# Kernel tuning notes

Measured on AMD Instinct MI355X. Metric: run time of the kernel, lower is better.

The kernel has to match this reference:

```python
import jax, jax.numpy as jnp
import numpy as np

# --- quantization helpers (I-BERT-style symmetric quantization) ---

def _quant_int(x, scale, bit):
    # round(x/scale) clamped to signed `bit`-bit range (SymmetricQuantFunction)
    n = 2 ** (bit - 1) - 1
    return jnp.clip(jnp.round(x / scale), -n - 1, n)


def quant_linear(x, s_x, W, b, weight_bit=8):
    """QuantLinear: per-output-channel symmetric 8-bit weight quant, int GEMM, dequant.
    Returns (output, bias_scaling_factor[out_features])."""
    n = 2 ** (weight_bit - 1) - 1
    w_scale = jnp.maximum(jnp.max(jnp.abs(W), axis=1), 1e-8) / n          # (out,)
    w_int = _quant_int(W, w_scale[:, None], weight_bit)                   # int-valued (out,in)
    b_scale = w_scale * s_x                                               # (out,) broadcasts with scalar s_x
    b_int = jnp.round(b / b_scale)                                        # 32-bit bias, no clamp needed
    x_int = x / s_x                                                       # int-valued activations
    out_int = jnp.einsum('bsi,oi->bso', x_int, w_int) + b_int
    return out_int * b_scale, b_scale


def quant_act(x, bit):
    """QuantAct: per-tensor symmetric requantization to `bit` bits (dynamic min/max)."""
    n = 2 ** (bit - 1) - 1
    scale = jnp.maximum(jnp.max(jnp.abs(x)), 1e-8) / n                    # scalar
    x_int = _quant_int(x, scale, bit)
    return x_int * scale, scale


def int_gelu(x, s):
    """IntGELU (I-BERT): integer 2nd-order polynomial approximation of erf."""
    k = 1.4142
    c0, c1 = -0.2888, -1.769
    c2 = 1.0 / c0
    SHIFT = 14  # 'const' in the original code

    x_int = x / s
    se = s / k  # scaling factor fed to int_erf
    # --- int_erf ---
    b_int = jnp.floor(c1 / se)
    c_int = jnp.floor(c2 / se ** 2)
    sign = jnp.sign(x_int)
    abs_int = jnp.minimum(jnp.abs(x_int), -b_int)
    y_int = sign * ((abs_int + b_int) ** 2 + c_int)
    se2 = se ** 2 * c0
    y_int = jnp.floor(y_int / 2 ** SHIFT)
    se2 = se2 * 2 ** SHIFT
    # --- gelu = x * (erf/2 + 1/2) in integer form ---
    shift_int = jnp.floor(1.0 / se2)
    out_int = x_int * (y_int + shift_int)
    s_out = s * se2 / 2
    return out_int * s_out, s_out


def setup_inputs() -> dict:
    key = jax.random.key(0)
    k_x, k_w1, k_b1, k_w2, k_b2 = jax.random.split(key, 5)
    B, S, D, H = 8, 1024, 768, 3072
    x = jax.random.normal(k_x, (B, S, D), dtype=jnp.float32)
    act_scaling_factor = jnp.full((1,), 0.02, dtype=jnp.float32)
    # pre-quantize x onto its input grid (x arrives already quantized in the real pipeline)
    x = jnp.round(x / act_scaling_factor) * act_scaling_factor
    W1 = jax.random.normal(k_w1, (H, D), dtype=jnp.float32) * 0.02
    b1 = jax.random.normal(k_b1, (H,), dtype=jnp.float32) * 0.02
    W2 = jax.random.normal(k_w2, (D, H), dtype=jnp.float32) * 0.02
    b2 = jax.random.normal(k_b2, (D,), dtype=jnp.float32) * 0.02
    return {"x": x, "act_scaling_factor": act_scaling_factor,
            "W1": W1, "b1": b1, "W2": W2, "b2": b2}


def reference(x, act_scaling_factor, W1, b1, W2, b2):
    s = act_scaling_factor
    h, s = quant_linear(x, s, W1, b1)       # fc1: int8 GEMM + dequant
    h, s = quant_act(h, 8)                  # qact_gelu
    h, s = int_gelu(h, s)                   # IntGELU
    h, s = quant_act(h, 8)                  # qact1 (drop=0.0 -> identity)
    h, s = quant_linear(h, s, W2, b2)       # fc2
    h, s = quant_act(h, 16)                 # qact2 (16-bit)
    return h, s
```

## Files before the change

### kernel.cpp

```cpp
#include <hip/hip_runtime.h>

typedef _Float16 half8  __attribute__((ext_vector_type(8)));
typedef _Float16 half4v __attribute__((ext_vector_type(4)));
typedef float f32x4 __attribute__((ext_vector_type(4)));
typedef int int4v __attribute__((ext_vector_type(4)));

#define M_DIM 8192
#define D_DIM 768
#define H_DIM 3072

#define WS_WSCALE2   16
#define WS_BINT1     (WS_WSCALE2 + 768*4)
#define WS_BSCALE1   (WS_BINT1 + 3072*4)
#define WS_BINT2     (WS_BSCALE1 + 3072*4)
#define WS_BSCALE2   (WS_BINT2 + 768*4)
#define WS_XQ        34560UL
#define WS_WQ1       (WS_XQ  + (size_t)M_DIM*D_DIM*2)
#define WS_WQ2I      (WS_WQ1 + (size_t)H_DIM*D_DIM*2)
#define WS_H1        (WS_WQ2I + (size_t)D_DIM*H_DIM)
#define WS_Q2        WS_H1
#define WS_H2        (WS_H1 + (size_t)M_DIM*H_DIM)
#define WS_Q1        (WS_H1 + (size_t)M_DIM*H_DIM*4)

__device__ __forceinline__ void gl_lds16(const _Float16* g, _Float16* l) {
  __builtin_amdgcn_global_load_lds(
      (const __attribute__((address_space(1))) void*)g,
      (__attribute__((address_space(3))) void*)l, 16, 0, 0);
}
__device__ __forceinline__ void gl_lds16c(const char* g, char* l) {
  __builtin_amdgcn_global_load_lds(
      (const __attribute__((address_space(1))) void*)g,
      (__attribute__((address_space(3))) void*)l, 16, 0, 0);
}

struct GeluP { float scale1, bintg, cintg, shiftint, s_out; };

__device__ __forceinline__ GeluP gelu_params(float max1) {
  GeluP p;
  p.scale1 = fmaxf(max1, 1e-8f) / 127.0f;
  float se = p.scale1 / 1.4142f;
  p.bintg = floorf(-1.769f / se);
  p.cintg = floorf(((float)(1.0 / -0.2888)) / (se * se));
  float se2 = ((se * se) * -0.2888f) * 16384.0f;
  p.shiftint = floorf(1.0f / se2);
  p.s_out = (p.scale1 * se2) * 0.5f;
  return p;
}

__device__ __forceinline__ float gelu_val(const GeluP& p, float qf) {
  float sg = (qf > 0.f) ? 1.f : ((qf < 0.f) ? -1.f : 0.f);
  float aq = fminf(fabsf(qf), -p.bintg);
  float t = aq + p.bintg;
  float y = sg * (t * t + p.cintg);
  float yf = floorf(y * (1.0f / 16384.0f));
  return (qf * (yf + p.shiftint)) * p.s_out;
}

__global__ __launch_bounds__(256)
void k1_prep(const float* __restrict__ W1, const float* __restrict__ b1,
             const float* __restrict__ W2, const float* __restrict__ sxp,
             _Float16* __restrict__ wq1, char* __restrict__ wq2i,
             float* __restrict__ wscale2, float* __restrict__ bint1,
             float* __restrict__ bscale1, unsigned* __restrict__ wsu)
{
  if (blockIdx.x == 0 && threadIdx.x == 0) { wsu[0] = 0u; wsu[1] = 0u; wsu[2] = 0u; }
  int w = blockIdx.x * 4 + (threadIdx.x >> 6);
  int lane = threadIdx.x & 63;
  if (w < H_DIM) {
    const float* row = W1 + (size_t)w * D_DIM;
    f32x4 v[3]; float m = 0.f;
#pragma unroll
    for (int t = 0; t < 3; t++) {
      v[t] = *(const f32x4*)(row + t * 256 + lane * 4);
#pragma unroll
      for (int j = 0; j < 4; j++) m = fmaxf(m, fabsf(v[t][j]));
    }
#pragma unroll
    for (int off = 32; off >= 1; off >>= 1) m = fmaxf(m, __shfl_xor(m, off));
    float wsc = fmaxf(m, 1e-8f) / 127.0f;
    _Float16* orow = wq1 + (size_t)w * D_DIM;
#pragma unroll
    for (int t = 0; t < 3; t++) {
      half4v h;
#pragma unroll
      for (int j = 0; j < 4; j++) {
        float q = fminf(fmaxf(rintf(v[t][j] / wsc), -128.f), 127.f);
        h[j] = (_Float16)q;
      }
      *(half4v*)(orow + t * 256 + lane * 4) = h;
    }
    if (lane == 0) {
      float bs = wsc * sxp[0];
      bint1[w] = rintf(b1[w] / bs);
      bscale1[w] = bs;
    }
  } else {
    int o = w - H_DIM;
    const float* row = W2 + (size_t)o * H_DIM;
    f32x4 v[12]; float m = 0.f;
#pragma unroll
    for (int t = 0; t < 12; t++) {
      v[t] = *(const f32x4*)(row + t * 256 + lane * 4);
#pragma unroll
      for (int j = 0; j < 4; j++) m = fmaxf(m, fabsf(v[t][j]));
    }
#pragma unroll
    for (int off = 32; off >= 1; off >>= 1) m = fmaxf(m, __shfl_xor(m, off));
    float wsc = fmaxf(m, 1e-8f) / 127.0f;
    unsigned* orow = (unsigned*)(wq2i + (size_t)o * H_DIM);
#pragma unroll
    for (int t = 0; t < 12; t++) {
      unsigned pk = 0;
#pragma unroll
      for (int j = 0; j < 4; j++) {
        float q = fminf(fmaxf(rintf(v[t][j] / wsc), -128.f), 127.f);
        pk |= ((unsigned)(unsigned char)(char)(int)q) << (8 * j);
      }
      orow[t * 64 + lane] = pk;
    }
    if (lane == 0) wscale2[o] = wsc;
  }
}

__global__ __launch_bounds__(256)
void k2_quant_x(const float* __restrict__ x, const float* __restrict__ sxp,
                _Float16* __restrict__ xq, int n4)
{
  float sx = sxp[0];
  int stride = gridDim.x * blockDim.x;
  for (int i = blockIdx.x * blockDim.x + threadIdx.x; i < n4; i += stride) {
    f32x4 v = ((const f32x4*)x)[i];
    half4v h;
#pragma unroll
    for (int j = 0; j < 4; j++) h[j] = (_Float16)(v[j] / sx);
    ((half4v*)xq)[i] = h;
  }
}

#define SLOT_A 4096
#define SLOT_B 8192
#define SLOT_SZ (SLOT_A + SLOT_B)

__global__ __launch_bounds__(512)
void gemm_f16_dp(const _Float16* __restrict__ A, const _Float16* __restrict__ B,
                 const float* __restrict__ bint, const float* __restrict__ bscale,
                 float* __restrict__ C, unsigned* __restrict__ maxw, int N, int K)
{
  __shared__ _Float16 lds[3 * SLOT_SZ];
  __shared__ float wred[8];
  const int tid = threadIdx.x;
  const int wid = tid >> 6;
  const int lane = tid & 63;
  const int m0 = blockIdx.x * 128;
  const int n0 = blockIdx.y * 256;
  const int wm = wid >> 2;
  const int wn = wid & 3;

  const int sr = lane >> 2;
  const int sc = lane & 3;
  const int ra  = wid * 16 + sr;
  const int csa = sc ^ ((ra >> 1) & 3);
  const int rb  = wid * 16 + sr;
  const int csb = sc ^ ((rb >> 1) & 3);
  const _Float16* pa  = A + (size_t)(m0 + ra) * K + csa * 8;
  const _Float16* pb0 = B + (size_t)(n0 + rb) * K + csb * 8;
  const _Float16* pb1 = B + (size_t)(n0 + rb + 128) * K + csb * 8;
  _Float16* const da  = lds;
  _Float16* const db0 = lds + SLOT_A;
  _Float16* const db1 = lds + SLOT_A + 4096;

#define STAGE_DP(t, s) do {                                                  \
    const int _o = (s) * SLOT_SZ + wid * 512;                                \
    gl_lds16(pa  + (size_t)(t) * 32, da  + _o);                              \
    gl_lds16(pb0 + (size_t)(t) * 32, db0 + _o);                              \
    gl_lds16(pb1 + (size_t)(t) * 32, db1 + _o);                              \
  } while (0)

  int aoff[4], boff[4];
  const int ks = lane >> 4;
#pragma unroll
  for (int f = 0; f < 4; f++) {
    int r = wm * 64 + f * 16 + (lane & 15);
    aoff[f] = r * 64 + ((ks ^ ((r >> 1) & 3)) * 16);
    int rn = wn * 64 + f * 16 + (lane & 15);
    boff[f] = SLOT_A * 2 + rn * 64 + ((ks ^ ((rn >> 1) & 3)) * 16);
  }

  f32x4 acc[4][4];
#pragma unroll
  for (int i = 0; i < 4; i++)
#pragma unroll
    for (int j = 0; j < 4; j++) acc[i][j] = (f32x4){0.f, 0.f, 0.f, 0.f};

  const int nt = K / 32;
  STAGE_DP(0, 0);
  STAGE_DP(1, 1);
  for (int t = 0; t < nt; ++t) {
    const int s = t % 3;
    if (t + 1 < nt) asm volatile("s_waitcnt vmcnt(3)" ::: "memory");
    else            asm volatile("s_waitcnt vmcnt(0)" ::: "memory");
    asm volatile("s_barrier" ::: "memory");
    if (t + 2 < nt) STAGE_DP(t + 2, (t + 2) % 3);
    const char* sb = (const char*)(lds + s * SLOT_SZ);
    half8 a[4], b01[2], b23[2];
#pragma unroll
    for (int f = 0; f < 4; f++) a[f] = *(const half8*)(sb + aoff[f]);
    b01[0] = *(const half8*)(sb + boff[0]);
    b01[1] = *(const half8*)(sb + boff[1]);
    __builtin_amdgcn_s_setprio(1);
#pragma unroll
    for (int i = 0; i < 4; i++)
#pragma unroll
      for (int j = 0; j < 2; j++)
        acc[i][j] = __builtin_amdgcn_mfma_f32_16x16x32_f16(a[i], b01[j], acc[i][j], 0, 0, 0);
    __builtin_amdgcn_s_setprio(0);
    b23[0] = *(const half8*)(sb + boff[2]);
    b23[1] = *(const half8*)(sb + boff[3]);
    __builtin_amdgcn_s_setprio(1);
#pragma unroll
    for (int i = 0; i < 4; i++)
#pragma unroll
      for (int j = 0; j < 2; j++)
        acc[i][j + 2] = __builtin_amdgcn_mfma_f32_16x16x32_f16(a[i], b23[j], acc[i][j + 2], 0, 0, 0);
    __builtin_amdgcn_s_setprio(0);
  }
#undef STAGE_DP

  float tmax = 0.f;
  const int orow0 = m0 + wm * 64 + (lane >> 4) * 4;
  const int ocol0 = n0 + wn * 64 + (lane & 15);
#pragma unroll
  for (int j = 0; j < 4; j++) {
    const int col = ocol0 + j * 16;
    const float bi = bint[col];
    const float bs = bscale[col];
#pragma unroll
    for (int i = 0; i < 4; i++) {
#pragma unroll
      for (int e = 0; e < 4; e++) {
        const int rowm = orow0 + i * 16 + e;
        float v = (acc[i][j][e] + bi) * bs;
        C[(size_t)rowm * N + col] = v;
        tmax = fmaxf(tmax, fabsf(v));
      }
    }
  }
#pragma unroll
  for (int off = 32; off >= 1; off >>= 1) tmax = fmaxf(tmax, __shfl_xor(tmax, off));
  if (lane == 0) wred[wid] = tmax;
  __syncthreads();
  if (tid == 0) {
    float bm = 0.f;
#pragma unroll
    for (int i = 0; i < 8; i++) bm = fmaxf(bm, wred[i]);
    atomicMax(maxw, __float_as_uint(bm));
  }
}

__global__ __launch_bounds__(256)
void k4_gelu(const float* __restrict__ h1, const unsigned* __restrict__ wsu,
             char* __restrict__ q1, unsigned* __restrict__ maxw, int n4)
{
  GeluP p = gelu_params(__uint_as_float(wsu[0]));
  float tmax = 0.f;
  int stride = gridDim.x * blockDim.x;
  for (int i = blockIdx.x * blockDim.x + threadIdx.x; i < n4; i += stride) {
    f32x4 h = ((const f32x4*)h1)[i];
    unsigned pack = 0;
#pragma unroll
    for (int j = 0; j < 4; j++) {
      float qf = fminf(fmaxf(rintf(h[j] / p.scale1), -128.f), 127.f);
      tmax = fmaxf(tmax, fabsf(gelu_val(p, qf)));
      pack |= ((unsigned)(unsigned char)(char)(int)qf) << (8 * j);
    }
    ((unsigned*)q1)[i] = pack;
  }
#pragma unroll
  for (int off = 32; off >= 1; off >>= 1) tmax = fmaxf(tmax, __shfl_xor(tmax, off));
  __shared__ float wred[4];
  int wid = threadIdx.x >> 6;
  if ((threadIdx.x & 63) == 0) wred[wid] = tmax;
  __syncthreads();
  if (threadIdx.x == 0) {
    float bm = fmaxf(fmaxf(wred[0], wred[1]), fmaxf(wred[2], wred[3]));
    atomicMax(maxw, __float_as_uint(bm));
  }
}

__global__ __launch_bounds__(256)
void k6_bias(const unsigned* __restrict__ wsu, const float* __restrict__ wscale2,
             const float* __restrict__ b2, float* __restrict__ bint2,
             float* __restrict__ bscale2)
{
  float scale2 = fmaxf(__uint_as_float(wsu[1]), 1e-8f) / 127.0f;
  for (int o = threadIdx.x; o < D_DIM; o += 256) {
    float bs = wscale2[o] * scale2;
    bint2[o] = rintf(b2[o] / bs);
    bscale2[o] = bs;
  }
}

__global__ __launch_bounds__(256)
void k5_q2(const char* __restrict__ q1, const unsigned* __restrict__ wsu,
           char* __restrict__ q2, int n16)
{
  GeluP p = gelu_params(__uint_as_float(wsu[0]));
  float scale2 = fmaxf(__uint_as_float(wsu[1]), 1e-8f) / 127.0f;
  int stride = gridDim.x * blockDim.x;
  for (int i = blockIdx.x * blockDim.x + threadIdx.x; i < n16; i += stride) {
    uint4 pk = ((const uint4*)q1)[i];
    uint4 o;
    unsigned* pw[4] = {&o.x, &o.y, &o.z, &o.w};
    unsigned pr[4] = {pk.x, pk.y, pk.z, pk.w};
#pragma unroll
    for (int w = 0; w < 4; w++) {
      unsigned acc = 0;
#pragma unroll
      for (int j = 0; j < 4; j++) {
        float qf = (float)(int)(signed char)(pr[w] >> (8 * j));
        float g = gelu_val(p, qf);
        float q2f = fminf(fmaxf(rintf(g / scale2), -128.f), 127.f);
        acc |= ((unsigned)(unsigned char)(char)(int)q2f) << (8 * j);
      }
      *pw[w] = acc;
    }
    ((uint4*)q2)[i] = o;
  }
}

#define I8_SLOT_A 8192
#define I8_SLOT_SZ (2 * I8_SLOT_A)

__global__ __launch_bounds__(256)
void gemm_i8_dp(const char* __restrict__ A, const char* __restrict__ B,
                const float* __restrict__ bint, const float* __restrict__ bscale,
                float* __restrict__ C, unsigned* __restrict__ maxw, int N, int K)
{
  __shared__ char lds[3 * I8_SLOT_SZ];
  __shared__ float wred[4];
  const int tid = threadIdx.x;
  const int wid = tid >> 6;
  const int lane = tid & 63;
  const int m0 = blockIdx.x * 128;
  const int n0 = blockIdx.y * 128;
  const int wm = wid >> 1;
  const int wn = wid & 1;

  const int rr = lane >> 2;
  const int c  = lane & 3;
  const int r0 = wid * 16 + rr;
  const int r1 = r0 + 64;
  const int c0 = c ^ (r0 & 3) ^ ((r0 >> 2) & 3);
  const int c1 = c ^ (r1 & 3) ^ ((r1 >> 2) & 3);
  const char* pa0 = A + (size_t)(m0 + r0) * K + c0 * 16;
  const char* pa1 = A + (size_t)(m0 + r1) * K + c1 * 16;
  const char* pb0 = B + (size_t)(n0 + r0) * K + c0 * 16;
  const char* pb1 = B + (size_t)(n0 + r1) * K + c1 * 16;

#define STAGE_I8(t, s) do {                                                   \
    char* const base = lds + (s) * I8_SLOT_SZ;                                \
    gl_lds16c(pa0 + (size_t)(t) * 64, base + wid * 1024);                     \
    gl_lds16c(pa1 + (size_t)(t) * 64, base + 4096 + wid * 1024);              \
    gl_lds16c(pb0 + (size_t)(t) * 64, base + I8_SLOT_A + wid * 1024);         \
    gl_lds16c(pb1 + (size_t)(t) * 64, base + I8_SLOT_A + 4096 + wid * 1024);  \
  } while (0)

  int aoff[4], boff[4];
  const int ks = lane >> 4;
#pragma unroll
  for (int f = 0; f < 4; f++) {
    int r = wm * 64 + f * 16 + (lane & 15);
    aoff[f] = r * 64 + ((ks ^ (r & 3) ^ ((r >> 2) & 3)) * 16);
    int rn = wn * 64 + f * 16 + (lane & 15);
    boff[f] = I8_SLOT_A + rn * 64 + ((ks ^ (rn & 3) ^ ((rn >> 2) & 3)) * 16);
  }

  int4v acc[4][4];
#pragma unroll
  for (int i = 0; i < 4; i++)
#pragma unroll
    for (int j = 0; j < 4; j++) acc[i][j] = (int4v){0, 0, 0, 0};

  const int nt = K / 64;
  STAGE_I8(0, 0);
  STAGE_I8(1, 1);
  for (int t = 0; t < nt; ++t) {
    const int s = t % 3;
    if (t + 1 < nt) asm volatile("s_waitcnt vmcnt(4)" ::: "memory");
    else            asm volatile("s_waitcnt vmcnt(0)" ::: "memory");
    asm volatile("s_barrier" ::: "memory");
    if (t + 2 < nt) STAGE_I8(t + 2, (t + 2) % 3);
    const char* sb = lds + s * I8_SLOT_SZ;
    int4v a[4], b01[2], b23[2];
#pragma unroll
    for (int f = 0; f < 4; f++) a[f] = *(const int4v*)(sb + aoff[f]);
    b01[0] = *(const int4v*)(sb + boff[0]);
    b01[1] = *(const int4v*)(sb + boff[1]);
    __builtin_amdgcn_s_setprio(1);
#pragma unroll
    for (int i = 0; i < 4; i++)
#pragma unroll
      for (int j = 0; j < 2; j++)
        acc[i][j] = __builtin_amdgcn_mfma_i32_16x16x64_i8(a[i], b01[j], acc[i][j], 0, 0, 0);
    __builtin_amdgcn_s_setprio(0);
    b23[0] = *(const int4v*)(sb + boff[2]);
    b23[1] = *(const int4v*)(sb + boff[3]);
    __builtin_amdgcn_s_setprio(1);
#pragma unroll
    for (int i = 0; i < 4; i++)
#pragma unroll
      for (int j = 0; j < 2; j++)
        acc[i][j + 2] = __builtin_amdgcn_mfma_i32_16x16x64_i8(a[i], b23[j], acc[i][j + 2], 0, 0, 0);
    __builtin_amdgcn_s_setprio(0);
  }
#undef STAGE_I8

  float tmax = 0.f;
  const int orow0 = m0 + wm * 64 + (lane >> 4) * 4;
  const int ocol0 = n0 + wn * 64 + (lane & 15);
#pragma unroll
  for (int j = 0; j < 4; j++) {
    const int col = ocol0 + j * 16;
    const float bi = bint[col];
    const float bs = bscale[col];
#pragma unroll
    for (int i = 0; i < 4; i++) {
#pragma unroll
      for (int e = 0; e < 4; e++) {
        const int rowm = orow0 + i * 16 + e;
        float v = ((float)acc[i][j][e] + bi) * bs;
        C[(size_t)rowm * N + col] = v;
        tmax = fmaxf(tmax, fabsf(v));
      }
    }
  }
#pragma unroll
  for (int off = 32; off >= 1; off >>= 1) tmax = fmaxf(tmax, __shfl_xor(tmax, off));
  if (lane == 0) wred[wid] = tmax;
  __syncthreads();
  if (tid == 0) {
    float bm = fmaxf(fmaxf(wred[0], wred[1]), fmaxf(wred[2], wred[3]));
    atomicMax(maxw, __float_as_uint(bm));
  }
}

__global__ __launch_bounds__(256)
void k7_final(const float* __restrict__ h2, const unsigned* __restrict__ wsu,
              float* __restrict__ out, int n4, int ntot)
{
  float scale16 = fmaxf(__uint_as_float(wsu[2]), 1e-8f) / 32767.0f;
  int stride = gridDim.x * blockDim.x;
  for (int i = blockIdx.x * blockDim.x + threadIdx.x; i < n4; i += stride) {
    f32x4 v = ((const f32x4*)h2)[i];
    f32x4 o;
#pragma unroll
    for (int j = 0; j < 4; j++) {
      float q = fminf(fmaxf(rintf(v[j] / scale16), -32768.f), 32767.f);
      o[j] = q * scale16;
    }
    ((f32x4*)out)[i] = o;
  }
  if (blockIdx.x == 0 && threadIdx.x == 0) out[ntot] = scale16;
}

extern "C" void kernel_launch(void* const* d_in, const int* in_sizes, int n_in,
                              void* d_out, int out_size, void* d_ws, size_t ws_size,
                              hipStream_t stream)
{
  (void)in_sizes; (void)n_in; (void)out_size; (void)ws_size;
  const float* x  = (const float*)d_in[0];
  const float* sx = (const float*)d_in[1];
  const float* W1 = (const float*)d_in[2];
  const float* b1 = (const float*)d_in[3];
  const float* W2 = (const float*)d_in[4];
  const float* b2 = (const float*)d_in[5];
  float* out = (float*)d_out;
  char* ws = (char*)d_ws;

  unsigned* wsu   = (unsigned*)ws;
  float* wscale2  = (float*)(ws + WS_WSCALE2);
  float* bint1    = (float*)(ws + WS_BINT1);
  float* bscale1  = (float*)(ws + WS_BSCALE1);
  float* bint2    = (float*)(ws + WS_BINT2);
  float* bscale2  = (float*)(ws + WS_BSCALE2);
  _Float16* xq    = (_Float16*)(ws + WS_XQ);
  _Float16* wq1   = (_Float16*)(ws + WS_WQ1);
  char* wq2i      = (char*)(ws + WS_WQ2I);
  float* h1       = (float*)(ws + WS_H1);
  char* q2        = (char*)(ws + WS_Q2);
  float* h2       = (float*)(ws + WS_H2);
  char* q1        = (char*)(ws + WS_Q1);

  k1_prep<<<dim3(960), dim3(256), 0, stream>>>(W1, b1, W2, sx, wq1, wq2i, wscale2, bint1, bscale1, wsu);
  k2_quant_x<<<dim3(2048), dim3(256), 0, stream>>>(x, sx, xq, (M_DIM * D_DIM) / 4);
  gemm_f16_dp<<<dim3(64, 12), dim3(512), 0, stream>>>(xq, wq1, bint1, bscale1, h1, wsu + 0, H_DIM, D_DIM);
  k4_gelu<<<dim3(2048), dim3(256), 0, stream>>>(h1, wsu, q1, wsu + 1, (M_DIM * H_DIM) / 4);
  k6_bias<<<dim3(1), dim3(256), 0, stream>>>(wsu, wscale2, b2, bint2, bscale2);
  k5_q2<<<dim3(2048), dim3(256), 0, stream>>>(q1, wsu, q2, (M_DIM * H_DIM) / 16);
  gemm_i8_dp<<<dim3(64, 6), dim3(256), 0, stream>>>(q2, wq2i, bint2, bscale2, h2, wsu + 2, D_DIM, H_DIM);
  k7_final<<<dim3(2048), dim3(256), 0, stream>>>(h2, wsu, out, (M_DIM * D_DIM) / 4, M_DIM * D_DIM);
}
```

Baseline: 183.4 us.

## Fuse GELU requant into int8 GEMM via LUT and merge prep kernels

Removes the separate q1->q2 requantization pass and the bias kernel by building a 256-entry GELU+requant lookup table per wave from shuffled registers. The second GEMM's A operand is loaded to registers, remapped through the table, and written to LDS, while B keeps the direct global-to-LDS path. The bias is computed in the epilogue, and the weight prep and x quantization kernels are merged into one launch. The GEMM tile shrinks to 64 rows to fit the register-staged A path, which doubles the grid but lowers per-block reuse of B and adds shuffle work to the inner loop.

```diff
diff --git a/kernel.cpp b/kernel.cpp
--- a/kernel.cpp
+++ b/kernel.cpp
@@ -12,13 +12,10 @@
 #define WS_WSCALE2   16
 #define WS_BINT1     (WS_WSCALE2 + 768*4)
 #define WS_BSCALE1   (WS_BINT1 + 3072*4)
-#define WS_BINT2     (WS_BSCALE1 + 3072*4)
-#define WS_BSCALE2   (WS_BINT2 + 768*4)
 #define WS_XQ        34560UL
 #define WS_WQ1       (WS_XQ  + (size_t)M_DIM*D_DIM*2)
 #define WS_WQ2I      (WS_WQ1 + (size_t)H_DIM*D_DIM*2)
 #define WS_H1        (WS_WQ2I + (size_t)D_DIM*H_DIM)
-#define WS_Q2        WS_H1
 #define WS_H2        (WS_H1 + (size_t)M_DIM*H_DIM)
 #define WS_Q1        (WS_H1 + (size_t)M_DIM*H_DIM*4)
 
@@ -57,83 +54,83 @@
 }
 
 __global__ __launch_bounds__(256)
-void k1_prep(const float* __restrict__ W1, const float* __restrict__ b1,
-             const float* __restrict__ W2, const float* __restrict__ sxp,
-             _Float16* __restrict__ wq1, char* __restrict__ wq2i,
-             float* __restrict__ wscale2, float* __restrict__ bint1,
-             float* __restrict__ bscale1, unsigned* __restrict__ wsu)
+void k12_prep(const float* __restrict__ W1, const float* __restrict__ b1,
+              const float* __restrict__ W2, const float* __restrict__ x,
+              const float* __restrict__ sxp,
+              _Float16* __restrict__ wq1, char* __restrict__ wq2i,
+              float* __restrict__ wscale2, float* __restrict__ bint1,
+              float* __restrict__ bscale1, _Float16* __restrict__ xq,
+              unsigned* __restrict__ wsu)
 {
   if (blockIdx.x == 0 && threadIdx.x == 0) { wsu[0] = 0u; wsu[1] = 0u; wsu[2] = 0u; }
-  int w = blockIdx.x * 4 + (threadIdx.x >> 6);
-  int lane = threadIdx.x & 63;
-  if (w < H_DIM) {
-    const float* row = W1 + (size_t)w * D_DIM;
-    f32x4 v[3]; float m = 0.f;
-#pragma unroll
-    for (int t = 0; t < 3; t++) {
-      v[t] = *(const f32x4*)(row + t * 256 + lane * 4);
-#pragma unroll
-      for (int j = 0; j < 4; j++) m = fmaxf(m, fabsf(v[t][j]));
-    }
-#pragma unroll
-    for (int off = 32; off >= 1; off >>= 1) m = fmaxf(m, __shfl_xor(m, off));
-    float wsc = fmaxf(m, 1e-8f) / 127.0f;
-    _Float16* orow = wq1 + (size_t)w * D_DIM;
-#pragma unroll
-    for (int t = 0; t < 3; t++) {
+  if (blockIdx.x < 960) {
+    int w = blockIdx.x * 4 + (threadIdx.x >> 6);
+    int lane = threadIdx.x & 63;
+    if (w < H_DIM) {
+      const float* row = W1 + (size_t)w * D_DIM;
+      f32x4 v[3]; float m = 0.f;
+#pragma unroll
+      for (int t = 0; t < 3; t++) {
+        v[t] = *(const f32x4*)(row + t * 256 + lane * 4);
+#pragma unroll
+        for (int j = 0; j < 4; j++) m = fmaxf(m, fabsf(v[t][j]));
+      }
+#pragma unroll
+      for (int off = 32; off >= 1; off >>= 1) m = fmaxf(m, __shfl_xor(m, off));
+      float wsc = fmaxf(m, 1e-8f) / 127.0f;
+      _Float16* orow = wq1 + (size_t)w * D_DIM;
+#pragma unroll
+      for (int t = 0; t < 3; t++) {
+        half4v h;
+#pragma unroll
+        for (int j = 0; j < 4; j++) {
+          float q = fminf(fmaxf(rintf(v[t][j] / wsc), -128.f), 127.f);
+          h[j] = (_Float16)q;
+        }
+        *(half4v*)(orow + t * 256 + lane * 4) = h;
+      }
+      if (lane == 0) {
+        float bs = wsc * sxp[0];
+        bint1[w] = rintf(b1[w] / bs);
+        bscale1[w] = bs;
+      }
+    } else {
+      int o = w - H_DIM;
+      const float* row = W2 + (size_t)o * H_DIM;
+      f32x4 v[12]; float m = 0.f;
+#pragma unroll
+      for (int t = 0; t < 12; t++) {
+        v[t] = *(const f32x4*)(row + t * 256 + lane * 4);
+#pragma unroll
+        for (int j = 0; j < 4; j++) m = fmaxf(m, fabsf(v[t][j]));
+      }
+#pragma unroll
+      for (int off = 32; off >= 1; off >>= 1) m = fmaxf(m, __shfl_xor(m, off));
+      float wsc = fmaxf(m, 1e-8f) / 127.0f;
+      unsigned* orow = (unsigned*)(wq2i + (size_t)o * H_DIM);
+#pragma unroll
+      for (int t = 0; t < 12; t++) {
+        unsigned pk = 0;
+#pragma unroll
+        for (int j = 0; j < 4; j++) {
+          float q = fminf(fmaxf(rintf(v[t][j] / wsc), -128.f), 127.f);
+          pk |= ((unsigned)(unsigned char)(char)(int)q) << (8 * j);
+        }
+        orow[t * 64 + lane] = pk;
+      }
+      if (lane == 0) wscale2[o] = wsc;
+    }
+  } else {
+    float sx = sxp[0];
+    const int n4 = (M_DIM * D_DIM) / 4;
+    const int stride = 1024 * 256;
+    for (int i = (blockIdx.x - 960) * 256 + threadIdx.x; i < n4; i += stride) {
+      f32x4 v = ((const f32x4*)x)[i];
       half4v h;
 #pragma unroll
-      for (int j = 0; j < 4; j++) {
-        float q = fminf(fmaxf(rintf(v[t][j] / wsc), -128.f), 127.f);
-        h[j] = (_Float16)q;
-      }
-      *(half4v*)(orow + t * 256 + lane * 4) = h;
-    }
-    if (lane == 0) {
-      float bs = wsc * sxp[0];
-      bint1[w] = rintf(b1[w] / bs);
-      bscale1[w] = bs;
-    }
-  } else {
-    int o = w - H_DIM;
-    const float* row = W2 + (size_t)o * H_DIM;
-    f32x4 v[12]; float m = 0.f;
-#pragma unroll
-    for (int t = 0; t < 12; t++) {
-      v[t] = *(const f32x4*)(row + t * 256 + lane * 4);
-#pragma unroll
-      for (int j = 0; j < 4; j++) m = fmaxf(m, fabsf(v[t][j]));
-    }
-#pragma unroll
-    for (int off = 32; off >= 1; off >>= 1) m = fmaxf(m, __shfl_xor(m, off));
-    float wsc = fmaxf(m, 1e-8f) / 127.0f;
-    unsigned* orow = (unsigned*)(wq2i + (size_t)o * H_DIM);
-#pragma unroll
-    for (int t = 0; t < 12; t++) {
-      unsigned pk = 0;
-#pragma unroll
-      for (int j = 0; j < 4; j++) {
-        float q = fminf(fmaxf(rintf(v[t][j] / wsc), -128.f), 127.f);
-        pk |= ((unsigned)(unsigned char)(char)(int)q) << (8 * j);
-      }
-      orow[t * 64 + lane] = pk;
-    }
-    if (lane == 0) wscale2[o] = wsc;
-  }
-}
-
-__global__ __launch_bounds__(256)
-void k2_quant_x(const float* __restrict__ x, const float* __restrict__ sxp,
-                _Float16* __restrict__ xq, int n4)
-{
-  float sx = sxp[0];
-  int stride = gridDim.x * blockDim.x;
-  for (int i = blockIdx.x * blockDim.x + threadIdx.x; i < n4; i += stride) {
-    f32x4 v = ((const f32x4*)x)[i];
-    half4v h;
-#pragma unroll
-    for (int j = 0; j < 4; j++) h[j] = (_Float16)(v[j] / sx);
-    ((half4v*)xq)[i] = h;
+      for (int j = 0; j < 4; j++) h[j] = (_Float16)(v[j] / sx);
+      ((half4v*)xq)[i] = h;
+    }
   }
 }
 
@@ -287,118 +284,127 @@
   }
 }
 
+#define I8L_SLOT 12288
+
 __global__ __launch_bounds__(256)
-void k6_bias(const unsigned* __restrict__ wsu, const float* __restrict__ wscale2,
-             const float* __restrict__ b2, float* __restrict__ bint2,
-             float* __restrict__ bscale2)
+void gemm_i8_lut(const char* __restrict__ q1, const char* __restrict__ B,
+                 const unsigned* __restrict__ wsu, const float* __restrict__ wscale2,
+                 const float* __restrict__ b2, float* __restrict__ C,
+                 unsigned* __restrict__ maxw, int N, int K)
 {
-  float scale2 = fmaxf(__uint_as_float(wsu[1]), 1e-8f) / 127.0f;
-  for (int o = threadIdx.x; o < D_DIM; o += 256) {
-    float bs = wscale2[o] * scale2;
-    bint2[o] = rintf(b2[o] / bs);
-    bscale2[o] = bs;
-  }
-}
-
-__global__ __launch_bounds__(256)
-void k5_q2(const char* __restrict__ q1, const unsigned* __restrict__ wsu,
-           char* __restrict__ q2, int n16)
-{
-  GeluP p = gelu_params(__uint_as_float(wsu[0]));
-  float scale2 = fmaxf(__uint_as_float(wsu[1]), 1e-8f) / 127.0f;
-  int stride = gridDim.x * blockDim.x;
-  for (int i = blockIdx.x * blockDim.x + threadIdx.x; i < n16; i += stride) {
-    uint4 pk = ((const uint4*)q1)[i];
-    uint4 o;
-    unsigned* pw[4] = {&o.x, &o.y, &o.z, &o.w};
-    unsigned pr[4] = {pk.x, pk.y, pk.z, pk.w};
-#pragma unroll
-    for (int w = 0; w < 4; w++) {
-      unsigned acc = 0;
-#pragma unroll
-      for (int j = 0; j < 4; j++) {
-        float qf = (float)(int)(signed char)(pr[w] >> (8 * j));
-        float g = gelu_val(p, qf);
-        float q2f = fminf(fmaxf(rintf(g / scale2), -128.f), 127.f);
-        acc |= ((unsigned)(unsigned char)(char)(int)q2f) << (8 * j);
-      }
-      *pw[w] = acc;
-    }
-    ((uint4*)q2)[i] = o;
-  }
-}
-
-#define I8_SLOT_A 8192
-#define I8_SLOT_SZ (2 * I8_SLOT_A)
-
-__global__ __launch_bounds__(256)
-void gemm_i8_dp(const char* __restrict__ A, const char* __restrict__ B,
-                const float* __restrict__ bint, const float* __restrict__ bscale,
-                float* __restrict__ C, unsigned* __restrict__ maxw, int N, int K)
-{
-  __shared__ char lds[3 * I8_SLOT_SZ];
+  __shared__ char lds[3 * I8L_SLOT];
   __shared__ float wred[4];
   const int tid = threadIdx.x;
   const int wid = tid >> 6;
   const int lane = tid & 63;
-  const int m0 = blockIdx.x * 128;
+  const int m0 = blockIdx.x * 64;
   const int n0 = blockIdx.y * 128;
   const int wm = wid >> 1;
   const int wn = wid & 1;
 
-  const int rr = lane >> 2;
-  const int c  = lane & 3;
-  const int r0 = wid * 16 + rr;
-  const int r1 = r0 + 64;
-  const int c0 = c ^ (r0 & 3) ^ ((r0 >> 2) & 3);
-  const int c1 = c ^ (r1 & 3) ^ ((r1 >> 2) & 3);
-  const char* pa0 = A + (size_t)(m0 + r0) * K + c0 * 16;
-  const char* pa1 = A + (size_t)(m0 + r1) * K + c1 * 16;
-  const char* pb0 = B + (size_t)(n0 + r0) * K + c0 * 16;
-  const char* pb1 = B + (size_t)(n0 + r1) * K + c1 * 16;
-
-#define STAGE_I8(t, s) do {                                                   \
-    char* const base = lds + (s) * I8_SLOT_SZ;                                \
-    gl_lds16c(pa0 + (size_t)(t) * 64, base + wid * 1024);                     \
-    gl_lds16c(pa1 + (size_t)(t) * 64, base + 4096 + wid * 1024);              \
-    gl_lds16c(pb0 + (size_t)(t) * 64, base + I8_SLOT_A + wid * 1024);         \
-    gl_lds16c(pb1 + (size_t)(t) * 64, base + I8_SLOT_A + 4096 + wid * 1024);  \
+  GeluP p = gelu_params(__uint_as_float(wsu[0]));
+  const float scale2 = fmaxf(__uint_as_float(wsu[1]), 1e-8f) / 127.0f;
+  unsigned lutw = 0;
+#pragma unroll
+  for (int j = 0; j < 4; j++) {
+    float qf = (float)(lane * 4 + j - 128);
+    float g = gelu_val(p, qf);
+    float q2f = fminf(fmaxf(rintf(g / scale2), -128.f), 127.f);
+    lutw |= ((unsigned)(unsigned char)(char)(int)q2f) << (8 * j);
+  }
+
+  const int sr = tid >> 2;
+  const int sc = tid & 3;
+  const int csw = sc ^ ((sr >> 1) & 3);
+  const char* paq = q1 + (size_t)(m0 + sr) * K + sc * 16;
+  const int awaddr = sr * 64 + csw * 16;
+  const char* pb0 = B + (size_t)(n0 + sr) * K + csw * 16;
+  const char* pb1 = B + (size_t)(n0 + 64 + sr) * K + csw * 16;
+
+#define STAGE_B(t, s) do {                                                   \
+    char* const base = lds + (s) * I8L_SLOT + 4096 + wid * 1024;             \
+    gl_lds16c(pb0 + (size_t)(t) * 64, base);                                 \
+    gl_lds16c(pb1 + (size_t)(t) * 64, base + 4096);                          \
   } while (0)
 
-  int aoff[4], boff[4];
+  int aoff[2], boff[4];
   const int ks = lane >> 4;
 #pragma unroll
+  for (int f = 0; f < 2; f++) {
+    int r = wm * 32 + f * 16 + (lane & 15);
+    aoff[f] = r * 64 + ((ks ^ ((r >> 1) & 3)) * 16);
+  }
+#pragma unroll
   for (int f = 0; f < 4; f++) {
-    int r = wm * 64 + f * 16 + (lane & 15);
-    aoff[f] = r * 64 + ((ks ^ (r & 3) ^ ((r >> 2) & 3)) * 16);
     int rn = wn * 64 + f * 16 + (lane & 15);
-    boff[f] = I8_SLOT_A + rn * 64 + ((ks ^ (rn & 3) ^ ((rn >> 2) & 3)) * 16);
-  }
-
-  int4v acc[4][4];
-#pragma unroll
-  for (int i = 0; i < 4; i++)
+    boff[f] = 4096 + rn * 64 + ((ks ^ ((rn >> 1) & 3)) * 16);
+  }
+
+  int4v acc[2][4];
+#pragma unroll
+  for (int i = 0; i < 2; i++)
 #pragma unroll
     for (int j = 0; j < 4; j++) acc[i][j] = (int4v){0, 0, 0, 0};
 
   const int nt = K / 64;
-  STAGE_I8(0, 0);
-  STAGE_I8(1, 1);
+
+  uint4 ar0 = *(const uint4*)(paq);
+  STAGE_B(0, 0);
+  uint4 arn = *(const uint4*)(paq + 64);
+  STAGE_B(1, 1);
+  asm volatile("s_waitcnt vmcnt(3)" ::: "memory");
+  {
+    uint4 aw;
+    unsigned* s = (unsigned*)&ar0; unsigned* d = (unsigned*)&aw;
+#pragma unroll
+    for (int w = 0; w < 4; w++) {
+      unsigned r = 0;
+#pragma unroll
+      for (int j = 0; j < 4; j++) {
+        int idx = ((int)(signed char)(s[w] >> (8 * j))) + 128;
+        unsigned wd = (unsigned)__shfl((int)lutw, idx >> 2, 64);
+        r |= ((wd >> ((idx & 3) * 8)) & 0xFFu) << (8 * j);
+      }
+      d[w] = r;
+    }
+    *(uint4*)(lds + awaddr) = aw;
+  }
+
   for (int t = 0; t < nt; ++t) {
     const int s = t % 3;
-    if (t + 1 < nt) asm volatile("s_waitcnt vmcnt(4)" ::: "memory");
+    if (t + 1 < nt) asm volatile("s_waitcnt vmcnt(2)" ::: "memory");
     else            asm volatile("s_waitcnt vmcnt(0)" ::: "memory");
+    asm volatile("s_waitcnt lgkmcnt(0)" ::: "memory");
     asm volatile("s_barrier" ::: "memory");
-    if (t + 2 < nt) STAGE_I8(t + 2, (t + 2) % 3);
-    const char* sb = lds + s * I8_SLOT_SZ;
-    int4v a[4], b01[2], b23[2];
-#pragma unroll
-    for (int f = 0; f < 4; f++) a[f] = *(const int4v*)(sb + aoff[f]);
+    if (t + 1 < nt) {
+      uint4 aw;
+      unsigned* sp = (unsigned*)&arn; unsigned* d = (unsigned*)&aw;
+#pragma unroll
+      for (int w = 0; w < 4; w++) {
+        unsigned r = 0;
+#pragma unroll
+        for (int j = 0; j < 4; j++) {
+          int idx = ((int)(signed char)(sp[w] >> (8 * j))) + 128;
+          unsigned wd = (unsigned)__shfl((int)lutw, idx >> 2, 64);
+          r |= ((wd >> ((idx & 3) * 8)) & 0xFFu) << (8 * j);
+        }
+        d[w] = r;
+      }
+      *(uint4*)(lds + ((t + 1) % 3) * I8L_SLOT + awaddr) = aw;
+    }
+    if (t + 2 < nt) {
+      arn = *(const uint4*)(paq + (size_t)(t + 2) * 64);
+      STAGE_B(t + 2, (t + 2) % 3);
+    }
+    const char* sb = lds + s * I8L_SLOT;
+    int4v a[2], b01[2], b23[2];
+#pragma unroll
+    for (int f = 0; f < 2; f++) a[f] = *(const int4v*)(sb + aoff[f]);
     b01[0] = *(const int4v*)(sb + boff[0]);
     b01[1] = *(const int4v*)(sb + boff[1]);
     __builtin_amdgcn_s_setprio(1);
 #pragma unroll
-    for (int i = 0; i < 4; i++)
+    for (int i = 0; i < 2; i++)
 #pragma unroll
       for (int j = 0; j < 2; j++)
         acc[i][j] = __builtin_amdgcn_mfma_i32_16x16x64_i8(a[i], b01[j], acc[i][j], 0, 0, 0);
@@ -407,24 +413,24 @@
     b23[1] = *(const int4v*)(sb + boff[3]);
     __builtin_amdgcn_s_setprio(1);
 #pragma unroll
-    for (int i = 0; i < 4; i++)
+    for (int i = 0; i < 2; i++)
 #pragma unroll
       for (int j = 0; j < 2; j++)
         acc[i][j + 2] = __builtin_amdgcn_mfma_i32_16x16x64_i8(a[i], b23[j], acc[i][j + 2], 0, 0, 0);
     __builtin_amdgcn_s_setprio(0);
   }
-#undef STAGE_I8
+#undef STAGE_B
 
   float tmax = 0.f;
-  const int orow0 = m0 + wm * 64 + (lane >> 4) * 4;
+  const int orow0 = m0 + wm * 32 + (lane >> 4) * 4;
   const int ocol0 = n0 + wn * 64 + (lane & 15);
 #pragma unroll
   for (int j = 0; j < 4; j++) {
     const int col = ocol0 + j * 16;
-    const float bi = bint[col];
-    const float bs = bscale[col];
-#pragma unroll
-    for (int i = 0; i < 4; i++) {
+    const float bs = wscale2[col] * scale2;
+    const float bi = rintf(b2[col] / bs);
+#pragma unroll
+    for (int i = 0; i < 2; i++) {
 #pragma unroll
       for (int e = 0; e < 4; e++) {
         const int rowm = orow0 + i * 16 + e;
@@ -481,22 +487,17 @@
   float* wscale2  = (float*)(ws + WS_WSCALE2);
   float* bint1    = (float*)(ws + WS_BINT1);
   float* bscale1  = (float*)(ws + WS_BSCALE1);
-  float* bint2    = (float*)(ws + WS_BINT2);
-  float* bscale2  = (float*)(ws + WS_BSCALE2);
   _Float16* xq    = (_Float16*)(ws + WS_XQ);
   _Float16* wq1   = (_Float16*)(ws + WS_WQ1);
   char* wq2i      = (char*)(ws + WS_WQ2I);
   float* h1       = (float*)(ws + WS_H1);
-  char* q2        = (char*)(ws + WS_Q2);
   float* h2       = (float*)(ws + WS_H2);
   char* q1        = (char*)(ws + WS_Q1);
 
-  k1_prep<<<dim3(960), dim3(256), 0, stream>>>(W1, b1, W2, sx, wq1, wq2i, wscale2, bint1, bscale1, wsu);
-  k2_quant_x<<<dim3(2048), dim3(256), 0, stream>>>(x, sx, xq, (M_DIM * D_DIM) / 4);
+  k12_prep<<<dim3(1984), dim3(256), 0, stream>>>(W1, b1, W2, x, sx, wq1, wq2i,
+                                                 wscale2, bint1, bscale1, xq, wsu);
   gemm_f16_dp<<<dim3(64, 12), dim3(512), 0, stream>>>(xq, wq1, bint1, bscale1, h1, wsu + 0, H_DIM, D_DIM);
   k4_gelu<<<dim3(2048), dim3(256), 0, stream>>>(h1, wsu, q1, wsu + 1, (M_DIM * H_DIM) / 4);
-  k6_bias<<<dim3(1), dim3(256), 0, stream>>>(wsu, wscale2, b2, bint2, bscale2);
-  k5_q2<<<dim3(2048), dim3(256), 0, stream>>>(q1, wsu, q2, (M_DIM * H_DIM) / 16);
-  gemm_i8_dp<<<dim3(64, 6), dim3(256), 0, stream>>>(q2, wq2i, bint2, bscale2, h2, wsu + 2, D_DIM, H_DIM);
+  gemm_i8_lut<<<dim3(128, 6), dim3(256), 0, stream>>>(q1, wq2i, wsu, wscale2, b2, h2, wsu + 2, D_DIM, H_DIM);
   k7_final<<<dim3(2048), dim3(256), 0, stream>>>(h2, wsu, out, (M_DIM * D_DIM) / 4, M_DIM * D_DIM);
 }
```

Result: faster. 178.7 us (-2.6%).

## Fuse prep kernels, fold fc2 bias into int8 GEMM, retile GEMM to 64x192

Applied to the files above, without the earlier changes.

Merges the weight-quantization and x-quantization kernels into one launch by partitioning blocks, and removes the single-block fc2 bias kernel by computing bias scale and integer bias in the int8 GEMM epilogue. The int8 GEMM is retiled from 128x128 tiles (64x6 grid) to 64x192 tiles (128x4 grid), with each wave owning 48 columns and a new LDS swizzle. The goal is fewer launches and better CU coverage for fc2 (512 blocks instead of 384), at the cost of lower per-block A reuse and some redundant per-column bias math.

```diff
diff --git a/kernel.cpp b/kernel.cpp
--- a/kernel.cpp
+++ b/kernel.cpp
@@ -12,8 +12,6 @@
 #define WS_WSCALE2   16
 #define WS_BINT1     (WS_WSCALE2 + 768*4)
 #define WS_BSCALE1   (WS_BINT1 + 3072*4)
-#define WS_BINT2     (WS_BSCALE1 + 3072*4)
-#define WS_BSCALE2   (WS_BINT2 + 768*4)
 #define WS_XQ        34560UL
 #define WS_WQ1       (WS_XQ  + (size_t)M_DIM*D_DIM*2)
 #define WS_WQ2I      (WS_WQ1 + (size_t)H_DIM*D_DIM*2)
@@ -57,83 +55,83 @@
 }
 
 __global__ __launch_bounds__(256)
-void k1_prep(const float* __restrict__ W1, const float* __restrict__ b1,
-             const float* __restrict__ W2, const float* __restrict__ sxp,
-             _Float16* __restrict__ wq1, char* __restrict__ wq2i,
-             float* __restrict__ wscale2, float* __restrict__ bint1,
-             float* __restrict__ bscale1, unsigned* __restrict__ wsu)
+void k12_prep(const float* __restrict__ W1, const float* __restrict__ b1,
+              const float* __restrict__ W2, const float* __restrict__ x,
+              const float* __restrict__ sxp,
+              _Float16* __restrict__ wq1, char* __restrict__ wq2i,
+              float* __restrict__ wscale2, float* __restrict__ bint1,
+              float* __restrict__ bscale1, _Float16* __restrict__ xq,
+              unsigned* __restrict__ wsu)
 {
   if (blockIdx.x == 0 && threadIdx.x == 0) { wsu[0] = 0u; wsu[1] = 0u; wsu[2] = 0u; }
-  int w = blockIdx.x * 4 + (threadIdx.x >> 6);
-  int lane = threadIdx.x & 63;
-  if (w < H_DIM) {
-    const float* row = W1 + (size_t)w * D_DIM;
-    f32x4 v[3]; float m = 0.f;
-#pragma unroll
-    for (int t = 0; t < 3; t++) {
-      v[t] = *(const f32x4*)(row + t * 256 + lane * 4);
-#pragma unroll
-      for (int j = 0; j < 4; j++) m = fmaxf(m, fabsf(v[t][j]));
-    }
-#pragma unroll
-    for (int off = 32; off >= 1; off >>= 1) m = fmaxf(m, __shfl_xor(m, off));
-    float wsc = fmaxf(m, 1e-8f) / 127.0f;
-    _Float16* orow = wq1 + (size_t)w * D_DIM;
-#pragma unroll
-    for (int t = 0; t < 3; t++) {
+  if (blockIdx.x < 960) {
+    int w = blockIdx.x * 4 + (threadIdx.x >> 6);
+    int lane = threadIdx.x & 63;
+    if (w < H_DIM) {
+      const float* row = W1 + (size_t)w * D_DIM;
+      f32x4 v[3]; float m = 0.f;
+#pragma unroll
+      for (int t = 0; t < 3; t++) {
+        v[t] = *(const f32x4*)(row + t * 256 + lane * 4);
+#pragma unroll
+        for (int j = 0; j < 4; j++) m = fmaxf(m, fabsf(v[t][j]));
+      }
+#pragma unroll
+      for (int off = 32; off >= 1; off >>= 1) m = fmaxf(m, __shfl_xor(m, off));
+      float wsc = fmaxf(m, 1e-8f) / 127.0f;
+      _Float16* orow = wq1 + (size_t)w * D_DIM;
+#pragma unroll
+      for (int t = 0; t < 3; t++) {
+        half4v h;
+#pragma unroll
+        for (int j = 0; j < 4; j++) {
+          float q = fminf(fmaxf(rintf(v[t][j] / wsc), -128.f), 127.f);
+          h[j] = (_Float16)q;
+        }
+        *(half4v*)(orow + t * 256 + lane * 4) = h;
+      }
+      if (lane == 0) {
+        float bs = wsc * sxp[0];
+        bint1[w] = rintf(b1[w] / bs);
+        bscale1[w] = bs;
+      }
+    } else {
+      int o = w - H_DIM;
+      const float* row = W2 + (size_t)o * H_DIM;
+      f32x4 v[12]; float m = 0.f;
+#pragma unroll
+      for (int t = 0; t < 12; t++) {
+        v[t] = *(const f32x4*)(row + t * 256 + lane * 4);
+#pragma unroll
+        for (int j = 0; j < 4; j++) m = fmaxf(m, fabsf(v[t][j]));
+      }
+#pragma unroll
+      for (int off = 32; off >= 1; off >>= 1) m = fmaxf(m, __shfl_xor(m, off));
+      float wsc = fmaxf(m, 1e-8f) / 127.0f;
+      unsigned* orow = (unsigned*)(wq2i + (size_t)o * H_DIM);
+#pragma unroll
+      for (int t = 0; t < 12; t++) {
+        unsigned pk = 0;
+#pragma unroll
+        for (int j = 0; j < 4; j++) {
+          float q = fminf(fmaxf(rintf(v[t][j] / wsc), -128.f), 127.f);
+          pk |= ((unsigned)(unsigned char)(char)(int)q) << (8 * j);
+        }
+        orow[t * 64 + lane] = pk;
+      }
+      if (lane == 0) wscale2[o] = wsc;
+    }
+  } else {
+    float sx = sxp[0];
+    const int n4 = (M_DIM * D_DIM) / 4;
+    const int stride = 1024 * 256;
+    for (int i = (blockIdx.x - 960) * 256 + threadIdx.x; i < n4; i += stride) {
+      f32x4 v = ((const f32x4*)x)[i];
       half4v h;
 #pragma unroll
-      for (int j = 0; j < 4; j++) {
-        float q = fminf(fmaxf(rintf(v[t][j] / wsc), -128.f), 127.f);
-        h[j] = (_Float16)q;
-      }
-      *(half4v*)(orow + t * 256 + lane * 4) = h;
-    }
-    if (lane == 0) {
-      float bs = wsc * sxp[0];
-      bint1[w] = rintf(b1[w] / bs);
-      bscale1[w] = bs;
-    }
-  } else {
-    int o = w - H_DIM;
-    const float* row = W2 + (size_t)o * H_DIM;
-    f32x4 v[12]; float m = 0.f;
-#pragma unroll
-    for (int t = 0; t < 12; t++) {
-      v[t] = *(const f32x4*)(row + t * 256 + lane * 4);
-#pragma unroll
-      for (int j = 0; j < 4; j++) m = fmaxf(m, fabsf(v[t][j]));
-    }
-#pragma unroll
-    for (int off = 32; off >= 1; off >>= 1) m = fmaxf(m, __shfl_xor(m, off));
-    float wsc = fmaxf(m, 1e-8f) / 127.0f;
-    unsigned* orow = (unsigned*)(wq2i + (size_t)o * H_DIM);
-#pragma unroll
-    for (int t = 0; t < 12; t++) {
-      unsigned pk = 0;
-#pragma unroll
-      for (int j = 0; j < 4; j++) {
-        float q = fminf(fmaxf(rintf(v[t][j] / wsc), -128.f), 127.f);
-        pk |= ((unsigned)(unsigned char)(char)(int)q) << (8 * j);
-      }
-      orow[t * 64 + lane] = pk;
-    }
-    if (lane == 0) wscale2[o] = wsc;
-  }
-}
-
-__global__ __launch_bounds__(256)
-void k2_quant_x(const float* __restrict__ x, const float* __restrict__ sxp,
-                _Float16* __restrict__ xq, int n4)
-{
-  float sx = sxp[0];
-  int stride = gridDim.x * blockDim.x;
-  for (int i = blockIdx.x * blockDim.x + threadIdx.x; i < n4; i += stride) {
-    f32x4 v = ((const f32x4*)x)[i];
-    half4v h;
-#pragma unroll
-    for (int j = 0; j < 4; j++) h[j] = (_Float16)(v[j] / sx);
-    ((half4v*)xq)[i] = h;
+      for (int j = 0; j < 4; j++) h[j] = (_Float16)(v[j] / sx);
+      ((half4v*)xq)[i] = h;
+    }
   }
 }
 
@@ -288,19 +286,6 @@
 }
 
 __global__ __launch_bounds__(256)
-void k6_bias(const unsigned* __restrict__ wsu, const float* __restrict__ wscale2,
-             const float* __restrict__ b2, float* __restrict__ bint2,
-             float* __restrict__ bscale2)
-{
-  float scale2 = fmaxf(__uint_as_float(wsu[1]), 1e-8f) / 127.0f;
-  for (int o = threadIdx.x; o < D_DIM; o += 256) {
-    float bs = wscale2[o] * scale2;
-    bint2[o] = rintf(b2[o] / bs);
-    bscale2[o] = bs;
-  }
-}
-
-__global__ __launch_bounds__(256)
 void k5_q2(const char* __restrict__ q1, const unsigned* __restrict__ wsu,
            char* __restrict__ q2, int n16)
 {
@@ -328,101 +313,85 @@
   }
 }
 
-#define I8_SLOT_A 8192
-#define I8_SLOT_SZ (2 * I8_SLOT_A)
+#define I8_SLOT 16384
 
 __global__ __launch_bounds__(256)
 void gemm_i8_dp(const char* __restrict__ A, const char* __restrict__ B,
-                const float* __restrict__ bint, const float* __restrict__ bscale,
-                float* __restrict__ C, unsigned* __restrict__ maxw, int N, int K)
-{
-  __shared__ char lds[3 * I8_SLOT_SZ];
+                const unsigned* __restrict__ wsu, const float* __restrict__ wscale2,
+                const float* __restrict__ b2, float* __restrict__ C,
+                unsigned* __restrict__ maxw, int N, int K)
+{
+  __shared__ char lds[3 * I8_SLOT];
   __shared__ float wred[4];
   const int tid = threadIdx.x;
-  const int wid = tid >> 6;
-  const int lane = tid & 63;
-  const int m0 = blockIdx.x * 128;
-  const int n0 = blockIdx.y * 128;
-  const int wm = wid >> 1;
-  const int wn = wid & 1;
-
-  const int rr = lane >> 2;
-  const int c  = lane & 3;
-  const int r0 = wid * 16 + rr;
-  const int r1 = r0 + 64;
-  const int c0 = c ^ (r0 & 3) ^ ((r0 >> 2) & 3);
-  const int c1 = c ^ (r1 & 3) ^ ((r1 >> 2) & 3);
-  const char* pa0 = A + (size_t)(m0 + r0) * K + c0 * 16;
-  const char* pa1 = A + (size_t)(m0 + r1) * K + c1 * 16;
-  const char* pb0 = B + (size_t)(n0 + r0) * K + c0 * 16;
-  const char* pb1 = B + (size_t)(n0 + r1) * K + c1 * 16;
-
-#define STAGE_I8(t, s) do {                                                   \
-    char* const base = lds + (s) * I8_SLOT_SZ;                                \
-    gl_lds16c(pa0 + (size_t)(t) * 64, base + wid * 1024);                     \
-    gl_lds16c(pa1 + (size_t)(t) * 64, base + 4096 + wid * 1024);              \
-    gl_lds16c(pb0 + (size_t)(t) * 64, base + I8_SLOT_A + wid * 1024);         \
-    gl_lds16c(pb1 + (size_t)(t) * 64, base + I8_SLOT_A + 4096 + wid * 1024);  \
+  const int w = tid >> 6;
+  const int l = tid & 63;
+  const int m0 = blockIdx.x * 64;
+  const int n0 = blockIdx.y * 192;
+  const float scale2 = fmaxf(__uint_as_float(wsu[1]), 1e-8f) / 127.0f;
+
+  const int sri = l >> 2;
+  const int csw = (l & 3) ^ ((l >> 3) & 3);
+  const char* pa  = A + (size_t)(m0 + w * 16 + sri) * K + csw * 16;
+  const char* pbg = B + (size_t)(n0 + 48 * w + sri) * K + csw * 16;
+
+#define STAGE_I(t, s) do {                                                   \
+    char* const base = lds + (size_t)(s) * I8_SLOT;                          \
+    gl_lds16c(pa + (size_t)(t) * 64,                    base + w * 1024);    \
+    gl_lds16c(pbg + (size_t)(t) * 64,                   base + 4096 + (3*w) * 1024);     \
+    gl_lds16c(pbg + (size_t)16 * K + (size_t)(t) * 64,  base + 4096 + (3*w+1) * 1024);   \
+    gl_lds16c(pbg + (size_t)32 * K + (size_t)(t) * 64,  base + 4096 + (3*w+2) * 1024);   \
   } while (0)
 
-  int aoff[4], boff[4];
-  const int ks = lane >> 4;
-#pragma unroll
-  for (int f = 0; f < 4; f++) {
-    int r = wm * 64 + f * 16 + (lane & 15);
-    aoff[f] = r * 64 + ((ks ^ (r & 3) ^ ((r >> 2) & 3)) * 16);
-    int rn = wn * 64 + f * 16 + (lane & 15);
-    boff[f] = I8_SLOT_A + rn * 64 + ((ks ^ (rn & 3) ^ ((rn >> 2) & 3)) * 16);
-  }
-
-  int4v acc[4][4];
+  const int ks = l >> 4;
+  const int swc = (ks ^ (((l & 15) >> 1) & 3)) * 16;
+  int aoff[4], boff[3];
+#pragma unroll
+  for (int f = 0; f < 4; f++)
+    aoff[f] = (f * 16 + (l & 15)) * 64 + swc;
+#pragma unroll
+  for (int f = 0; f < 3; f++)
+    boff[f] = 4096 + ((3 * w + f) * 16 + (l & 15)) * 64 + swc;
+
+  int4v acc[4][3];
 #pragma unroll
   for (int i = 0; i < 4; i++)
 #pragma unroll
-    for (int j = 0; j < 4; j++) acc[i][j] = (int4v){0, 0, 0, 0};
+    for (int j = 0; j < 3; j++) acc[i][j] = (int4v){0, 0, 0, 0};
 
   const int nt = K / 64;
-  STAGE_I8(0, 0);
-  STAGE_I8(1, 1);
+  STAGE_I(0, 0);
+  STAGE_I(1, 1);
   for (int t = 0; t < nt; ++t) {
     const int s = t % 3;
     if (t + 1 < nt) asm volatile("s_waitcnt vmcnt(4)" ::: "memory");
     else            asm volatile("s_waitcnt vmcnt(0)" ::: "memory");
     asm volatile("s_barrier" ::: "memory");
-    if (t + 2 < nt) STAGE_I8(t + 2, (t + 2) % 3);
-    const char* sb = lds + s * I8_SLOT_SZ;
-    int4v a[4], b01[2], b23[2];
+    if (t + 2 < nt) STAGE_I(t + 2, (t + 2) % 3);
+    const char* sb = lds + (size_t)s * I8_SLOT;
+    int4v a[4], b[3];
 #pragma unroll
     for (int f = 0; f < 4; f++) a[f] = *(const int4v*)(sb + aoff[f]);
-    b01[0] = *(const int4v*)(sb + boff[0]);
-    b01[1] = *(const int4v*)(sb + boff[1]);
+#pragma unroll
+    for (int f = 0; f < 3; f++) b[f] = *(const int4v*)(sb + boff[f]);
     __builtin_amdgcn_s_setprio(1);
 #pragma unroll
     for (int i = 0; i < 4; i++)
 #pragma unroll
-      for (int j = 0; j < 2; j++)
-        acc[i][j] = __builtin_amdgcn_mfma_i32_16x16x64_i8(a[i], b01[j], acc[i][j], 0, 0, 0);
+      for (int j = 0; j < 3; j++)
+        acc[i][j] = __builtin_amdgcn_mfma_i32_16x16x64_i8(a[i], b[j], acc[i][j], 0, 0, 0);
     __builtin_amdgcn_s_setprio(0);
-    b23[0] = *(const int4v*)(sb + boff[2]);
-    b23[1] = *(const int4v*)(sb + boff[3]);
-    __builtin_amdgcn_s_setprio(1);
-#pragma unroll
-    for (int i = 0; i < 4; i++)
-#pragma unroll
-      for (int j = 0; j < 2; j++)
-        acc[i][j + 2] = __builtin_amdgcn_mfma_i32_16x16x64_i8(a[i], b23[j], acc[i][j + 2], 0, 0, 0);
-    __builtin_amdgcn_s_setprio(0);
-  }
-#undef STAGE_I8
+  }
+#undef STAGE_I
 
   float tmax = 0.f;
-  const int orow0 = m0 + wm * 64 + (lane >> 4) * 4;
-  const int ocol0 = n0 + wn * 64 + (lane & 15);
-#pragma unroll
-  for (int j = 0; j < 4; j++) {
+  const int orow0 = m0 + (l >> 4) * 4;
+  const int ocol0 = n0 + w * 48 + (l & 15);
+#pragma unroll
+  for (int j = 0; j < 3; j++) {
     const int col = ocol0 + j * 16;
-    const float bi = bint[col];
-    const float bs = bscale[col];
+    const float bs = wscale2[col] * scale2;
+    const float bi = rintf(b2[col] / bs);
 #pragma unroll
     for (int i = 0; i < 4; i++) {
 #pragma unroll
@@ -436,7 +405,7 @@
   }
 #pragma unroll
   for (int off = 32; off >= 1; off >>= 1) tmax = fmaxf(tmax, __shfl_xor(tmax, off));
-  if (lane == 0) wred[wid] = tmax;
+  if (l == 0) wred[w] = tmax;
   __syncthreads();
   if (tid == 0) {
     float bm = fmaxf(fmaxf(wred[0], wred[1]), fmaxf(wred[2], wred[3]));
@@ -481,8 +450,6 @@
   float* wscale2  = (float*)(ws + WS_WSCALE2);
   float* bint1    = (float*)(ws + WS_BINT1);
   float* bscale1  = (float*)(ws + WS_BSCALE1);
-  float* bint2    = (float*)(ws + WS_BINT2);
-  float* bscale2  = (float*)(ws + WS_BSCALE2);
   _Float16* xq    = (_Float16*)(ws + WS_XQ);
   _Float16* wq1   = (_Float16*)(ws + WS_WQ1);
   char* wq2i      = (char*)(ws + WS_WQ2I);
@@ -491,12 +458,11 @@
   float* h2       = (float*)(ws + WS_H2);
   char* q1        = (char*)(ws + WS_Q1);
 
-  k1_prep<<<dim3(960), dim3(256), 0, stream>>>(W1, b1, W2, sx, wq1, wq2i, wscale2, bint1, bscale1, wsu);
-  k2_quant_x<<<dim3(2048), dim3(256), 0, stream>>>(x, sx, xq, (M_DIM * D_DIM) / 4);
+  k12_prep<<<dim3(1984), dim3(256), 0, stream>>>(W1, b1, W2, x, sx, wq1, wq2i,
+                                                 wscale2, bint1, bscale1, xq, wsu);
   gemm_f16_dp<<<dim3(64, 12), dim3(512), 0, stream>>>(xq, wq1, bint1, bscale1, h1, wsu + 0, H_DIM, D_DIM);
   k4_gelu<<<dim3(2048), dim3(256), 0, stream>>>(h1, wsu, q1, wsu + 1, (M_DIM * H_DIM) / 4);
-  k6_bias<<<dim3(1), dim3(256), 0, stream>>>(wsu, wscale2, b2, bint2, bscale2);
   k5_q2<<<dim3(2048), dim3(256), 0, stream>>>(q1, wsu, q2, (M_DIM * H_DIM) / 16);
-  gemm_i8_dp<<<dim3(64, 6), dim3(256), 0, stream>>>(q2, wq2i, bint2, bscale2, h2, wsu + 2, D_DIM, H_DIM);
+  gemm_i8_dp<<<dim3(128, 4), dim3(256), 0, stream>>>(q2, wq2i, wsu, wscale2, b2, h2, wsu + 2, D_DIM, H_DIM);
   k7_final<<<dim3(2048), dim3(256), 0, stream>>>(h2, wsu, out, (M_DIM * D_DIM) / 4, M_DIM * D_DIM);
 }
```

New measurement: 178.9 us. 2.4% less time.
